# Kernel optimization log

Measured on AMD Instinct MI355X. Metric: run time of the kernel, lower is better.

## Reference

```python
import jax, jax.numpy as jnp
import numpy as np

DIM = 1024
HEADS = 16
BLK = 129
DK = 64
DV = 64
B = 4
N = BLK * 32  # 4128


def setup_inputs() -> dict:
    key = jax.random.key(0)
    ks = jax.random.split(key, 6)
    inner_k = HEADS * DK
    inner_v = HEADS * DV
    s = 1.0 / np.sqrt(DIM)
    x = jax.random.normal(ks[0], (B, N, DIM), dtype=jnp.float32)
    Wq = jax.random.normal(ks[1], (inner_k, DIM), dtype=jnp.float32) * s
    Wk = jax.random.normal(ks[2], (inner_k, DIM), dtype=jnp.float32) * s
    Wv = jax.random.normal(ks[3], (inner_v, DIM), dtype=jnp.float32) * s
    Wo = jax.random.normal(ks[4], (DIM, inner_v), dtype=jnp.float32) * (1.0 / np.sqrt(inner_v))
    bo = jax.random.normal(ks[5], (DIM,), dtype=jnp.float32) * 0.01
    return {"x": x, "Wq": Wq, "Wk": Wk, "Wv": Wv, "Wo": Wo, "bo": bo}


def reference(x, Wq, Wk, Wv, Wo, bo):
    Bsz, Nlen, D = x.shape
    nb = Nlen // BLK
    scale = 1.0 / np.sqrt(DK)
    # projections (Linear without bias: x @ W.T)
    q = (x @ Wq.T).reshape(Bsz, nb, BLK, HEADS, DK)
    k = (x @ Wk.T).reshape(Bsz, nb, BLK, HEADS, DK)
    v = (x @ Wv.T).reshape(Bsz, nb, BLK, HEADS, DV)
    # block-local attention: each block attends within itself
    scores = jnp.einsum('bnqhd,bnkhd->bnhqk', q, k) * scale  # [B,nb,H,BLK,BLK]
    attn = jax.nn.softmax(scores, axis=-1)
    out_blk = jnp.einsum('bnhqk,bnkhd->bnhqd', attn, v)  # [B,nb,H,BLK,DV]
    # global attention among the first token of each block
    qg = q[:, :, 0]  # [B,nb,H,DK]
    kg = k[:, :, 0]
    vg = v[:, :, 0]
    sg = jnp.einsum('bqhd,bkhd->bhqk', qg, kg) * scale  # [B,H,nb,nb]
    ag = jax.nn.softmax(sg, axis=-1)
    out_g = jnp.einsum('bhqk,bkhd->bqhd', ag, vg)  # [B,nb,H,DV]
    # add global output onto position 0 of each block
    out_blk = out_blk.at[:, :, :, 0, :].add(out_g.transpose(0, 1, 2, 3).swapaxes(2, 2))  # out_g already [B,nb,H,DV]
    # reassemble to [B,N,H*DV]
    out = out_blk.transpose(0, 1, 3, 2, 4).reshape(Bsz, Nlen, HEADS * DV)
    return out @ Wo.T + bo
```

## Files before the change

kernel.cpp:

```cpp
#include <hip/hip_runtime.h>

typedef unsigned short u16;
typedef __attribute__((ext_vector_type(8))) __bf16 bf16x8;
typedef __attribute__((ext_vector_type(4))) float f32x4;
typedef __attribute__((ext_vector_type(8))) u16 u16x8;
typedef __attribute__((ext_vector_type(4))) u16 u16x4;

#define DIMSZ 1024
#define HEADS 16
#define BLKSZ 129
#define NBLK 32
#define NTOK (BLKSZ * NBLK)
#define BATCH 4
#define MROWS (BATCH * NTOK)

#define MFMA __builtin_amdgcn_mfma_f32_16x16x32_bf16

#define SSTR 152
#define KSTR 72

#define NKT 32

__device__ __forceinline__ float bf2f(u16 u) {
  return __uint_as_float(((unsigned)u) << 16);
}
__device__ __forceinline__ u16 f2bf(float f) {
  unsigned u = __float_as_uint(f);
  u += 0x7FFFu + ((u >> 16) & 1u);
  return (u16)(u >> 16);
}

#define GLD16(ldsp, gp) __builtin_amdgcn_global_load_lds( \
    (const __attribute__((address_space(1))) void*)(gp),   \
    (__attribute__((address_space(3))) void*)(ldsp), 16, 0, 0)

__global__ __launch_bounds__(256) void cast_f32_bf16(
    const float* __restrict__ in, u16* __restrict__ out, int n)
{
  int i = (blockIdx.x * 256 + threadIdx.x) * 4;
  if (i < n) {
    float4 f = *(const float4*)(in + i);
    u16x4 o = { f2bf(f.x), f2bf(f.y), f2bf(f.z), f2bf(f.w) };
    *(u16x4*)(out + i) = o;
  }
}

__device__ __forceinline__ int xcd_swz(int bid, int nwg) {
  const int xcd = bid & 7, l = bid >> 3;
  const int q = nwg >> 3, r = nwg & 7;
  return (xcd < r ? xcd * (q + 1) : r * (q + 1) + (xcd - r) * q) + l;
}

__device__ __forceinline__ void stage_sq(u16* slot, const u16* gA,
                                         const u16* gB, int tid) {
  GLD16(slot + tid * 8, gA);
  GLD16(slot + 2048 + tid * 8, gA + 64 * DIMSZ);
  GLD16(slot + 4096 + tid * 8, gB);
  GLD16(slot + 6144 + tid * 8, gB + 64 * DIMSZ);
}

__device__ __forceinline__ void gemm_pipe_sq(
    const u16* __restrict__ A, const u16* __restrict__ Bm,
    int m0, int n0, int tid, u16 (*sm)[8192], f32x4 (*acc)[4])
{
  const int lane = tid & 63, w = tid >> 6;
  const int qd = lane >> 4, l15 = lane & 15;
  const int wm = (w >> 1) * 64, wn = (w & 1) * 64;
  const int qdsw = (qd ^ ((l15 >> 1) & 3)) * 8;

  const int srow = tid >> 2;
  const int schk = (tid & 3) ^ ((tid >> 3) & 3);
  const u16* gA = A + (size_t)(m0 + srow) * DIMSZ + schk * 8;
  const u16* gB = Bm + (size_t)(n0 + srow) * DIMSZ + schk * 8;

  stage_sq(sm[0], gA, gB, tid);
  stage_sq(sm[1], gA + 32, gB + 32, tid);
  asm volatile("s_waitcnt vmcnt(4)" ::: "memory");
  __builtin_amdgcn_s_barrier();
  __builtin_amdgcn_sched_barrier(0);

#pragma unroll 4
  for (int t = 0; t < NKT; ++t) {
    if (t + 2 < NKT)
      stage_sq(sm[(t + 2) & 3], gA + (t + 2) * 32, gB + (t + 2) * 32, tid);

    const u16* slot = sm[t & 3];
    bf16x8 af[4], bv[4];
#pragma unroll
    for (int mi = 0; mi < 4; ++mi)
      af[mi] = *(const bf16x8*)&slot[(wm + mi * 16 + l15) * 32 + qdsw];
#pragma unroll
    for (int ni = 0; ni < 4; ++ni)
      bv[ni] = *(const bf16x8*)&slot[4096 + (wn + ni * 16 + l15) * 32 + qdsw];

    __builtin_amdgcn_s_setprio(1);
#pragma unroll
    for (int mi = 0; mi < 4; ++mi)
#pragma unroll
      for (int ni = 0; ni < 4; ++ni)
        acc[mi][ni] = MFMA(af[mi], bv[ni], acc[mi][ni], 0, 0, 0);
    __builtin_amdgcn_s_setprio(0);

    __builtin_amdgcn_sched_barrier(0);
    if (t + 2 < NKT) {
      asm volatile("s_waitcnt vmcnt(4)" ::: "memory");
    } else {
      asm volatile("s_waitcnt vmcnt(0)" ::: "memory");
    }
    __builtin_amdgcn_s_barrier();
    __builtin_amdgcn_sched_barrier(0);
  }
}

__global__ __launch_bounds__(256, 2) void gemm_qkv(
    const u16* __restrict__ A, const u16* __restrict__ B,
    u16* __restrict__ Cq, u16* __restrict__ Ck, u16* __restrict__ Cv)
{
  __shared__ u16 sm[4][8192];
  const int tid = threadIdx.x;
  f32x4 acc[4][4];
#pragma unroll
  for (int mi = 0; mi < 4; ++mi)
#pragma unroll
    for (int ni = 0; ni < 4; ++ni)
      acc[mi][ni] = (f32x4){0.f, 0.f, 0.f, 0.f};

  const int wg = xcd_swz(blockIdx.x, 129 * 24);
  const int nt = wg % 24, mt = wg / 24;
  const int m0 = mt * 128, n0 = nt * 128;

  gemm_pipe_sq(A, B, m0, n0, tid, sm, acc);

  u16* C = nt < 8 ? Cq : (nt < 16 ? Ck : Cv);
  const int c0 = (nt & 7) * 128;
  const int lane = tid & 63, w = tid >> 6;
  const int qd = lane >> 4, l15 = lane & 15;
  const int wm = (w >> 1) * 64, wn = (w & 1) * 64;
#pragma unroll
  for (int mi = 0; mi < 4; ++mi)
#pragma unroll
    for (int ni = 0; ni < 4; ++ni) {
      const int row0 = m0 + wm + mi * 16 + qd * 4;
      const int col  = c0 + wn + ni * 16 + l15;
#pragma unroll
      for (int r = 0; r < 4; ++r)
        C[(size_t)(row0 + r) * DIMSZ + col] = f2bf(acc[mi][ni][r]);
    }
}

__global__ __launch_bounds__(256, 2) void gemm_out(
    const u16* __restrict__ A, const u16* __restrict__ B,
    float* __restrict__ C, const float* __restrict__ bias)
{
  __shared__ u16 sm[4][8192];
  const int tid = threadIdx.x;
  f32x4 acc[4][4];
#pragma unroll
  for (int mi = 0; mi < 4; ++mi)
#pragma unroll
    for (int ni = 0; ni < 4; ++ni)
      acc[mi][ni] = (f32x4){0.f, 0.f, 0.f, 0.f};

  const int wg = xcd_swz(blockIdx.x, 129 * 8);
  const int nt = wg & 7, mt = wg >> 3;
  const int m0 = mt * 128, n0 = nt * 128;

  gemm_pipe_sq(A, B, m0, n0, tid, sm, acc);

  const int lane = tid & 63, w = tid >> 6;
  const int qd = lane >> 4, l15 = lane & 15;
  const int wm = (w >> 1) * 64, wn = (w & 1) * 64;
#pragma unroll
  for (int mi = 0; mi < 4; ++mi)
#pragma unroll
    for (int ni = 0; ni < 4; ++ni) {
      const int row0 = m0 + wm + mi * 16 + qd * 4;
      const int col  = n0 + wn + ni * 16 + l15;
      float badd = bias[col];
#pragma unroll
      for (int r = 0; r < 4; ++r)
        C[(size_t)(row0 + r) * DIMSZ + col] = acc[mi][ni][r] + badd;
    }
}

__global__ __launch_bounds__(64) void global_attn(
    const u16* __restrict__ q, const u16* __restrict__ k,
    const u16* __restrict__ v, float* __restrict__ g)
{
  __shared__ float sQ[NBLK * 64];
  __shared__ float sKT[64 * NBLK];
  __shared__ float sV[NBLK * 64];
  __shared__ float sp[NBLK];
  const int b = blockIdx.x >> 4, h = blockIdx.x & 15;
  const int lane = threadIdx.x;

  for (int idx = lane; idx < NBLK * 64; idx += 64) {
    int j = idx >> 6, d = idx & 63;
    size_t off = ((size_t)(b * NTOK + j * BLKSZ)) * DIMSZ + h * 64 + d;
    sQ[idx] = bf2f(q[off]);
    sKT[d * NBLK + j] = bf2f(k[off]);
    sV[idx] = bf2f(v[off]);
  }
  __syncthreads();

  for (int i = 0; i < NBLK; ++i) {
    float s = -3.0e38f;
    if (lane < 32) {
      float acc = 0.f;
      for (int d = 0; d < 64; ++d) acc += sQ[i * 64 + d] * sKT[d * NBLK + lane];
      s = acc * 0.125f;
    }
    float m = s;
    for (int t = 1; t < 64; t <<= 1) m = fmaxf(m, __shfl_xor(m, t));
    float e = (lane < 32) ? __expf(s - m) : 0.f;
    float sum = e;
    for (int t = 1; t < 64; t <<= 1) sum += __shfl_xor(sum, t);
    if (lane < 32) sp[lane] = e / sum;
    __syncthreads();
    float acc = 0.f;
    for (int jj = 0; jj < NBLK; ++jj) acc += sp[jj] * sV[jj * 64 + lane];
    g[(((size_t)b * NBLK + i) * HEADS + h) * 64 + lane] = acc;
    __syncthreads();
  }
}

__global__ __launch_bounds__(512) void block_attn(
    const u16* q, const u16* __restrict__ k,
    const u16* __restrict__ v, const float* __restrict__ g,
    u16* ao)
{
  __shared__ u16 sS[144 * SSTR];
  __shared__ u16 sKV[144 * KSTR];
  const int b = blockIdx.x, blk = blockIdx.y, h = blockIdx.z;
  const int tid = threadIdx.x, lane = tid & 63, w = tid >> 6;
  const int qd = lane >> 4, l15 = lane & 15;
  const int h64 = h * 64;
  const size_t row_base = (size_t)b * NTOK + (size_t)blk * BLKSZ;
  const f32x4 zero4 = {0.f, 0.f, 0.f, 0.f};

  {
    const u16x8 zero8 = {0, 0, 0, 0, 0, 0, 0, 0};
    for (int c = tid; c < 144 * 8; c += 512) {
      int row = c >> 3, cc = c & 7;
      u16x8 val = zero8;
      if (row < BLKSZ)
        val = *(const u16x8*)(k + (row_base + row) * DIMSZ + h64 + cc * 8);
      *(u16x8*)&sKV[row * KSTR + cc * 8] = val;
    }
  }
  __syncthreads();

  {
    const int tbeg = w * 10;
    const int tend = (w == 7) ? 81 : tbeg + 10;
    int cur_mt = -1;
    bf16x8 qf0, qf1;
    for (int t = tbeg; t < tend; ++t) {
      int mt = t / 9, nt = t - mt * 9;
      if (mt != cur_mt) {
        cur_mt = mt;
        int qrow = mt * 16 + l15;
        if (qrow > 128) qrow = 128;
        const u16* qp = q + (row_base + qrow) * DIMSZ + h64;
        qf0 = *(const bf16x8*)(qp + qd * 8);
        qf1 = *(const bf16x8*)(qp + 32 + qd * 8);
      }
      bf16x8 kf0 = *(const bf16x8*)&sKV[(nt * 16 + l15) * KSTR + qd * 8];
      bf16x8 kf1 = *(const bf16x8*)&sKV[(nt * 16 + l15) * KSTR + 32 + qd * 8];
      f32x4 c = zero4;
      c = MFMA(qf0, kf0, c, 0, 0, 0);
      c = MFMA(qf1, kf1, c, 0, 0, 0);
      int r0 = mt * 16 + qd * 4, col = nt * 16 + l15;
#pragma unroll
      for (int r = 0; r < 4; ++r)
        sS[(r0 + r) * SSTR + col] = f2bf(c[r] * 0.125f);
    }
  }
  __syncthreads();

  for (int c = tid; c < BLKSZ * 8; c += 512) {
    int row = c >> 3, cc = c & 7;
    u16x8 val = *(const u16x8*)(v + (row_base + row) * DIMSZ + h64 + cc * 8);
#pragma unroll
    for (int jj = 0; jj < 8; ++jj)
      sKV[(cc * 8 + jj) * SSTR + row] = val[jj];
  }

  for (int row = w; row < BLKSZ; row += 8) {
    float x1 = bf2f(sS[row * SSTR + lane]);
    float x2 = bf2f(sS[row * SSTR + 64 + lane]);
    float x3 = (lane == 0) ? bf2f(sS[row * SSTR + 128]) : -3.0e38f;
    float m = fmaxf(fmaxf(x1, x2), x3);
    for (int t = 1; t < 64; t <<= 1) m = fmaxf(m, __shfl_xor(m, t));
    float e1 = __expf(x1 - m), e2 = __expf(x2 - m);
    float e3 = (lane == 0) ? __expf(x3 - m) : 0.f;
    float s = e1 + e2 + e3;
    for (int t = 1; t < 64; t <<= 1) s += __shfl_xor(s, t);
    float inv = 1.f / s;
    sS[row * SSTR + lane] = f2bf(e1 * inv);
    sS[row * SSTR + 64 + lane] = f2bf(e2 * inv);
    if (lane == 0) sS[row * SSTR + 128] = f2bf(e3 * inv);
  }
  __syncthreads();

  for (int t = w; t < 36; t += 8) {
    int mt = t >> 2, nt = t & 3;
    f32x4 c = zero4;
#pragma unroll
    for (int kk = 0; kk < 128; kk += 32) {
      bf16x8 pf = *(const bf16x8*)&sS[(mt * 16 + l15) * SSTR + kk + qd * 8];
      bf16x8 vf = *(const bf16x8*)&sKV[(nt * 16 + l15) * SSTR + kk + qd * 8];
      c = MFMA(pf, vf, c, 0, 0, 0);
    }
    int dv = nt * 16 + l15;
    float v128 = bf2f(sKV[dv * SSTR + 128]);
    int r0 = mt * 16 + qd * 4;
#pragma unroll
    for (int r = 0; r < 4; ++r) {
      int row = r0 + r;
      if (row < BLKSZ) {
        float p128 = bf2f(sS[row * SSTR + 128]);
        float val = c[r] + p128 * v128;
        if (row == 0)
          val += g[(((size_t)b * NBLK + blk) * HEADS + h) * 64 + dv];
        ao[(row_base + row) * DIMSZ + h64 + dv] = f2bf(val);
      }
    }
  }
}

extern "C" void kernel_launch(void* const* d_in, const int* in_sizes, int n_in,
                              void* d_out, int out_size, void* d_ws, size_t ws_size,
                              hipStream_t stream) {
  const float* x  = (const float*)d_in[0];
  const float* Wq = (const float*)d_in[1];
  const float* Wk = (const float*)d_in[2];
  const float* Wv = (const float*)d_in[3];
  const float* Wo = (const float*)d_in[4];
  const float* bo = (const float*)d_in[5];
  float* out = (float*)d_out;

  char* ws = (char*)d_ws;
  const size_t xb = (size_t)MROWS * DIMSZ * sizeof(u16);
  float* gb     = (float*)ws;
  u16*   qb     = (u16*)(ws + (1u << 20));
  u16*   x16    = (u16*)(ws + (1u << 20) + xb);
  u16*   Wqkv16 = (u16*)(ws + (1u << 20) + 2 * xb);
  u16*   Wo16   = x16;
  u16*   kb     = (u16*)d_out;
  u16*   vb     = (u16*)d_out + (size_t)MROWS * DIMSZ;

  const int nx = MROWS * DIMSZ;
  const int nw = DIMSZ * DIMSZ;
  cast_f32_bf16<<<nx / 1024, 256, 0, stream>>>(x,  x16, nx);
  cast_f32_bf16<<<nw / 1024, 256, 0, stream>>>(Wq, Wqkv16,          nw);
  cast_f32_bf16<<<nw / 1024, 256, 0, stream>>>(Wk, Wqkv16 + nw,     nw);
  cast_f32_bf16<<<nw / 1024, 256, 0, stream>>>(Wv, Wqkv16 + 2 * nw, nw);

  gemm_qkv<<<dim3(129 * 24), 256, 0, stream>>>(x16, Wqkv16, qb, kb, vb);

  cast_f32_bf16<<<nw / 1024, 256, 0, stream>>>(Wo, Wo16, nw);

  global_attn<<<dim3(BATCH * HEADS), 64, 0, stream>>>(qb, kb, vb, gb);
  block_attn<<<dim3(BATCH, NBLK, HEADS), 512, 0, stream>>>(qb, kb, vb, gb, qb);
  gemm_out<<<dim3(129 * 8), 256, 0, stream>>>(qb, Wo16, out, bo);
}
```

Before: 432.5 us.

## Use triple-buffered GEMM LDS for 3 WGs/CU, merge weight casts, parallelize global attention

The GEMM pipeline shrinks from four LDS slots to three rotating pointers, and launch bounds rise to three workgroups per CU. The aim is higher occupancy and latency hiding in the QKV and output projections. The three weight casts are merged into one launch, and global attention now runs four waves per block, each handling separate query rows, with no block-wide barriers. The tighter register budget may cause spills, and with only three slots the prefetch-two-ahead scheme could race on slot reuse.

```diff
diff --git a/kernel.cpp b/kernel.cpp
--- a/kernel.cpp
+++ b/kernel.cpp
@@ -45,6 +45,19 @@
   }
 }
 
+__global__ __launch_bounds__(256) void cast_w3(
+    const float* __restrict__ a, const float* __restrict__ b,
+    const float* __restrict__ c, u16* __restrict__ out)
+{
+  const int nw = DIMSZ * DIMSZ;
+  int i = (blockIdx.x * 256 + threadIdx.x) * 4;
+  const float* src = (i < nw) ? a : (i < 2 * nw ? b : c);
+  int j = (i < nw) ? i : (i < 2 * nw ? i - nw : i - 2 * nw);
+  float4 f = *(const float4*)(src + j);
+  u16x4 o = { f2bf(f.x), f2bf(f.y), f2bf(f.z), f2bf(f.w) };
+  *(u16x4*)(out + i) = o;
+}
+
 __device__ __forceinline__ int xcd_swz(int bid, int nwg) {
   const int xcd = bid & 7, l = bid >> 3;
   const int q = nwg >> 3, r = nwg & 7;
@@ -73,25 +86,25 @@
   const u16* gA = A + (size_t)(m0 + srow) * DIMSZ + schk * 8;
   const u16* gB = Bm + (size_t)(n0 + srow) * DIMSZ + schk * 8;
 
-  stage_sq(sm[0], gA, gB, tid);
-  stage_sq(sm[1], gA + 32, gB + 32, tid);
+  u16 *p0 = sm[0], *p1 = sm[1], *p2 = sm[2];
+
+  stage_sq(p0, gA, gB, tid);
+  stage_sq(p1, gA + 32, gB + 32, tid);
   asm volatile("s_waitcnt vmcnt(4)" ::: "memory");
   __builtin_amdgcn_s_barrier();
   __builtin_amdgcn_sched_barrier(0);
 
-#pragma unroll 4
   for (int t = 0; t < NKT; ++t) {
     if (t + 2 < NKT)
-      stage_sq(sm[(t + 2) & 3], gA + (t + 2) * 32, gB + (t + 2) * 32, tid);
-
-    const u16* slot = sm[t & 3];
+      stage_sq(p2, gA + (t + 2) * 32, gB + (t + 2) * 32, tid);
+
     bf16x8 af[4], bv[4];
 #pragma unroll
     for (int mi = 0; mi < 4; ++mi)
-      af[mi] = *(const bf16x8*)&slot[(wm + mi * 16 + l15) * 32 + qdsw];
+      af[mi] = *(const bf16x8*)&p0[(wm + mi * 16 + l15) * 32 + qdsw];
 #pragma unroll
     for (int ni = 0; ni < 4; ++ni)
-      bv[ni] = *(const bf16x8*)&slot[4096 + (wn + ni * 16 + l15) * 32 + qdsw];
+      bv[ni] = *(const bf16x8*)&p0[4096 + (wn + ni * 16 + l15) * 32 + qdsw];
 
     __builtin_amdgcn_s_setprio(1);
 #pragma unroll
@@ -109,14 +122,16 @@
     }
     __builtin_amdgcn_s_barrier();
     __builtin_amdgcn_sched_barrier(0);
-  }
-}
-
-__global__ __launch_bounds__(256, 2) void gemm_qkv(
+
+    u16* tmp = p0; p0 = p1; p1 = p2; p2 = tmp;
+  }
+}
+
+__global__ __launch_bounds__(256, 3) void gemm_qkv(
     const u16* __restrict__ A, const u16* __restrict__ B,
     u16* __restrict__ Cq, u16* __restrict__ Ck, u16* __restrict__ Cv)
 {
-  __shared__ u16 sm[4][8192];
+  __shared__ u16 sm[3][8192];
   const int tid = threadIdx.x;
   f32x4 acc[4][4];
 #pragma unroll
@@ -148,11 +163,11 @@
     }
 }
 
-__global__ __launch_bounds__(256, 2) void gemm_out(
+__global__ __launch_bounds__(256, 3) void gemm_out(
     const u16* __restrict__ A, const u16* __restrict__ B,
     float* __restrict__ C, const float* __restrict__ bias)
 {
-  __shared__ u16 sm[4][8192];
+  __shared__ u16 sm[3][8192];
   const int tid = threadIdx.x;
   f32x4 acc[4][4];
 #pragma unroll
@@ -183,18 +198,18 @@
     }
 }
 
-__global__ __launch_bounds__(64) void global_attn(
+__global__ __launch_bounds__(256) void global_attn(
     const u16* __restrict__ q, const u16* __restrict__ k,
     const u16* __restrict__ v, float* __restrict__ g)
 {
   __shared__ float sQ[NBLK * 64];
   __shared__ float sKT[64 * NBLK];
   __shared__ float sV[NBLK * 64];
-  __shared__ float sp[NBLK];
+  __shared__ float sp[4][NBLK];
   const int b = blockIdx.x >> 4, h = blockIdx.x & 15;
-  const int lane = threadIdx.x;
-
-  for (int idx = lane; idx < NBLK * 64; idx += 64) {
+  const int tid = threadIdx.x, lane = tid & 63, w = tid >> 6;
+
+  for (int idx = tid; idx < NBLK * 64; idx += 256) {
     int j = idx >> 6, d = idx & 63;
     size_t off = ((size_t)(b * NTOK + j * BLKSZ)) * DIMSZ + h * 64 + d;
     sQ[idx] = bf2f(q[off]);
@@ -203,7 +218,7 @@
   }
   __syncthreads();
 
-  for (int i = 0; i < NBLK; ++i) {
+  for (int i = w; i < NBLK; i += 4) {
     float s = -3.0e38f;
     if (lane < 32) {
       float acc = 0.f;
@@ -215,12 +230,11 @@
     float e = (lane < 32) ? __expf(s - m) : 0.f;
     float sum = e;
     for (int t = 1; t < 64; t <<= 1) sum += __shfl_xor(sum, t);
-    if (lane < 32) sp[lane] = e / sum;
-    __syncthreads();
+    if (lane < 32) sp[w][lane] = e / sum;
+    asm volatile("s_waitcnt lgkmcnt(0)" ::: "memory");
     float acc = 0.f;
-    for (int jj = 0; jj < NBLK; ++jj) acc += sp[jj] * sV[jj * 64 + lane];
+    for (int jj = 0; jj < NBLK; ++jj) acc += sp[w][jj] * sV[jj * 64 + lane];
     g[(((size_t)b * NBLK + i) * HEADS + h) * 64 + lane] = acc;
-    __syncthreads();
   }
 }
 
@@ -352,16 +366,14 @@
 
   const int nx = MROWS * DIMSZ;
   const int nw = DIMSZ * DIMSZ;
-  cast_f32_bf16<<<nx / 1024, 256, 0, stream>>>(x,  x16, nx);
-  cast_f32_bf16<<<nw / 1024, 256, 0, stream>>>(Wq, Wqkv16,          nw);
-  cast_f32_bf16<<<nw / 1024, 256, 0, stream>>>(Wk, Wqkv16 + nw,     nw);
-  cast_f32_bf16<<<nw / 1024, 256, 0, stream>>>(Wv, Wqkv16 + 2 * nw, nw);
+  cast_f32_bf16<<<nx / 1024, 256, 0, stream>>>(x, x16, nx);
+  cast_w3<<<3 * nw / 1024, 256, 0, stream>>>(Wq, Wk, Wv, Wqkv16);
 
   gemm_qkv<<<dim3(129 * 24), 256, 0, stream>>>(x16, Wqkv16, qb, kb, vb);
 
   cast_f32_bf16<<<nw / 1024, 256, 0, stream>>>(Wo, Wo16, nw);
 
-  global_attn<<<dim3(BATCH * HEADS), 64, 0, stream>>>(qb, kb, vb, gb);
+  global_attn<<<dim3(BATCH * HEADS), 256, 0, stream>>>(qb, kb, vb, gb);
   block_attn<<<dim3(BATCH, NBLK, HEADS), 512, 0, stream>>>(qb, kb, vb, gb, qb);
   gemm_out<<<dim3(129 * 8), 256, 0, stream>>>(qb, Wo16, out, bo);
 }
```

Result: faster. 400.1 us (-7.5%).
